# Performance work log

Measured on AMD Instinct MI355X. Metric: run time of the kernel, lower is better.

## Reference

```python
import jax, jax.numpy as jnp
import numpy as np

B, V, F, N = 4, 8192, 16384, 8192
EPS = 1e-3        # criterion eps
WEIGHT = 1000.0   # criterion weight


def setup_inputs() -> dict:
    key = jax.random.key(0)
    k1, k2, k3 = jax.random.split(key, 3)
    pred_pos = jax.random.normal(k1, (B, N, 3), jnp.float32)
    obstacle_pos = jax.random.normal(k2, (B, V, 3), jnp.float32)
    obstacle_faces = jax.random.randint(k3, (B, F, 3), 0, V)
    return {"pred_pos": pred_pos, "obstacle_pos": obstacle_pos,
            "obstacle_faces": obstacle_faces}


def _centers_normals(pos, faces):
    # pos: [V,3], faces: [F,3] -> face centers [F,3], unit face normals [F,3]
    tri = pos[faces]                                   # [F,3,3]
    centers = tri.mean(axis=1)                         # gather(...).mean(-2)
    n = jnp.cross(tri[:, 1] - tri[:, 0], tri[:, 2] - tri[:, 0])
    n = n / jnp.maximum(jnp.linalg.norm(n, axis=-1, keepdims=True), 1e-12)
    return centers, n


def reference(pred_pos, obstacle_pos, obstacle_faces):
    centers, normals = jax.vmap(_centers_normals)(obstacle_pos, obstacle_faces)
    # brute-force 1-NN: argmin_f ||p - c_f||^2 == argmin_f (||c_f||^2 - 2 p.c_f)
    c2 = jnp.sum(centers * centers, axis=-1)                     # [B,F]
    dots = jnp.einsum('bnd,bfd->bnf', pred_pos, centers)         # [B,N,F] big
    nn_idx = jnp.argmin(c2[:, None, :] - 2.0 * dots, axis=-1)    # [B,N]
    idx3 = jnp.broadcast_to(nn_idx[:, :, None], nn_idx.shape + (3,))
    nn_points = jnp.take_along_axis(centers, idx3, axis=1)       # [B,N,3]
    nn_normals = jnp.take_along_axis(normals, idx3, axis=1)      # [B,N,3]
    distance = jnp.sum((pred_pos - nn_points) * nn_normals, axis=-1)  # [B,N]
    interp = jnp.maximum(EPS - distance, 0.0)
    perc = jnp.mean((interp > 0).astype(jnp.float32))            # mean over B of per-example means (equal N)
    loss = jnp.mean(jnp.sum(interp ** 3, axis=-1)) * WEIGHT      # sum_i loss_i / B * weight
    return loss, perc
```

## Files before the change

kernel.cpp:

```cpp
#include <hip/hip_runtime.h>
#include <cstdint>

typedef __attribute__((ext_vector_type(8)))  short short8;
typedef __attribute__((ext_vector_type(16))) float floatx16;

constexpr int NB = 4;
constexpr int NV = 8192;
constexpr int NF = 16384;
constexpr int NP = 8192;
constexpr float F_EPS = 1e-3f;
constexpr float F_WEIGHT = 1000.0f;
constexpr float BIAS = 1e-3f;

constexpr int PT_TILES = NP / 32;
constexpr int FC_TILES = NF / 32;
constexpr int TPB = 256;
constexpr int FS = 16;
constexpr int SL_TILES = FC_TILES / FS;
constexpr int CH = 16;
constexpr int NCHUNK = SL_TILES / CH;
constexpr int PGB = 64;

union FragU { uint4 u; short8 s; };

__device__ inline unsigned f2bf(float f) {
    unsigned u = __float_as_uint(f);
    return (u + 0x7FFFu + ((u >> 16) & 1u)) >> 16;
}
__device__ inline float bf2f(unsigned h) { return __uint_as_float(h << 16); }
__device__ inline unsigned pk(unsigned lo, unsigned hi) {
    return (lo & 0xFFFFu) | (hi << 16);
}

__global__ void prep_kernel(const float* __restrict__ pred,
                            const float* __restrict__ pos,
                            const int*   __restrict__ faces,
                            uint4* __restrict__ a_frags,
                            uint4* __restrict__ b_frags,
                            float4* __restrict__ centers4,
                            float4* __restrict__ normals4,
                            unsigned* __restrict__ keys,
                            float* __restrict__ acc,
                            unsigned* __restrict__ tk) {
    int i = blockIdx.x * blockDim.x + threadIdx.x;
    if (i >= NB * NF) return;
    if (i < 2) acc[i] = 0.0f;
    if (i == 0) tk[0] = 0u;

    const unsigned ONE = 0x3F80u;

    {
        int b = i / NF, f = i & (NF - 1);
        const float* p = pos + (size_t)b * NV * 3;
        int i0 = faces[3 * (size_t)i], i1 = faces[3 * (size_t)i + 1], i2 = faces[3 * (size_t)i + 2];
        float ax = p[3 * i0], ay = p[3 * i0 + 1], az = p[3 * i0 + 2];
        float bx = p[3 * i1], by = p[3 * i1 + 1], bz = p[3 * i1 + 2];
        float cx = p[3 * i2], cy = p[3 * i2 + 1], cz = p[3 * i2 + 2];

        const float third = 1.0f / 3.0f;
        float mx = (ax + bx + cx) * third;
        float my = (ay + by + cy) * third;
        float mz = (az + bz + cz) * third;
        float c2 = mx * mx + my * my + mz * mz;

        float e1x = bx - ax, e1y = by - ay, e1z = bz - az;
        float e2x = cx - ax, e2y = cy - ay, e2z = cz - az;
        float nx = e1y * e2z - e1z * e2y;
        float ny = e1z * e2x - e1x * e2z;
        float nz = e1x * e2y - e1y * e2x;
        float len = sqrtf(nx * nx + ny * ny + nz * nz);
        float inv = 1.0f / fmaxf(len, 1e-12f);

        centers4[i] = make_float4(mx, my, mz, c2);
        normals4[i] = make_float4(nx * inv, ny * inv, nz * inv, 0.0f);

        unsigned bhx = f2bf(mx), bhy = f2bf(my), bhz = f2bf(mz);
        unsigned blx = f2bf(mx - bf2f(bhx)), bly = f2bf(my - bf2f(bhy)), blz = f2bf(mz - bf2f(bhz));
        unsigned c2h = f2bf(c2);
        unsigned c2l = f2bf(c2 - bf2f(c2h));

        int tile = f >> 5, n = f & 31;
        uint4* bb = b_frags + (size_t)(b * FC_TILES + tile) * 64;
        bb[n]      = make_uint4(pk(bhx, bhy), pk(bhz, bhx), pk(bhy, bhz), pk(blx, bly));
        bb[32 + n] = make_uint4(pk(blz, blx), pk(bly, blz), pk(c2h, c2l), pk(ONE, ONE));
    }

    if (i < NB * NP) {
        keys[i] = 0xFFFFFFFFu;
        int pb = i / NP, pn = i & (NP - 1);
        float x = pred[3 * (size_t)i], y = pred[3 * (size_t)i + 1], z = pred[3 * (size_t)i + 2];
        unsigned hx = f2bf(x), hy = f2bf(y), hz = f2bf(z);
        float rx = x - bf2f(hx), ry = y - bf2f(hy), rz = z - bf2f(hz);
        unsigned ahx = f2bf(-2.f * bf2f(hx)), ahy = f2bf(-2.f * bf2f(hy)), ahz = f2bf(-2.f * bf2f(hz));
        unsigned alx = f2bf(-2.f * rx), aly = f2bf(-2.f * ry), alz = f2bf(-2.f * rz);
        float p2 = x * x + y * y + z * z + BIAS;
        unsigned p2h = f2bf(p2);
        unsigned p2l = f2bf(p2 - bf2f(p2h));

        int tile = pn >> 5, m = pn & 31;
        uint4* ab = a_frags + (size_t)(pb * PT_TILES + tile) * 64;
        ab[m]      = make_uint4(pk(ahx, ahy), pk(ahz, alx), pk(aly, alz), pk(ahx, ahy));
        ab[32 + m] = make_uint4(pk(ahz, alx), pk(aly, alz), pk(ONE, ONE), pk(p2h, p2l));
    }
}

__global__ __launch_bounds__(TPB) void nn_kernel(
        const uint4* __restrict__ a_frags,
        const uint4* __restrict__ b_frags,
        unsigned* __restrict__ keys) {
    const int pg = blockIdx.x, sl = blockIdx.y, b = blockIdx.z;
    const int tid = threadIdx.x, wave = tid >> 6, lane = tid & 63;

    __shared__ uint4 sb[CH * 64];

    const int pt_tile = pg * 4 + wave;
    FragU a;
    a.u = a_frags[((size_t)(b * PT_TILES + pt_tile)) * 64 + lane];

    unsigned best[16];
#pragma unroll
    for (int e = 0; e < 16; ++e) best[e] = 0xFFFFFFFFu;

    const floatx16 zero = {0.f, 0.f, 0.f, 0.f, 0.f, 0.f, 0.f, 0.f,
                           0.f, 0.f, 0.f, 0.f, 0.f, 0.f, 0.f, 0.f};
    const uint4* bp = b_frags + ((size_t)(b * FC_TILES + sl * SL_TILES)) * 64;

    for (int ch = 0; ch < NCHUNK; ++ch) {
        const uint4* gsrc = bp + (size_t)ch * CH * 64;
        __syncthreads();
#pragma unroll
        for (int k = 0; k < (CH * 64) / TPB; ++k)
            sb[k * TPB + tid] = gsrc[k * TPB + tid];
        __syncthreads();

        unsigned vf = (unsigned)((sl * SL_TILES + ch * CH) * 32 + (lane & 31));
#pragma unroll
        for (int t = 0; t < CH; t += 2) {
            FragU fb0, fb1;
            fb0.u = sb[t * 64 + lane];
            fb1.u = sb[t * 64 + 64 + lane];
            floatx16 d0, d1;
            asm("v_mfma_f32_32x32x16_bf16 %0, %2, %3, %5\n\t"
                "v_mfma_f32_32x32x16_bf16 %1, %2, %4, %5\n\t"
                "s_nop 7\n\t"
                "s_nop 7"
                : "=&v"(d0), "=&v"(d1)
                : "v"(a.s), "v"(fb0.s), "v"(fb1.s), "v"(zero));
#pragma unroll
            for (int r = 0; r < 16; ++r) {
                unsigned k0 = (__float_as_uint(d0[r]) & 0xFFFFC000u) | vf;
                unsigned k1 = (__float_as_uint(d1[r]) & 0xFFFFC000u) | (vf + 32u);
                best[r] = min(best[r], min(k0, k1));
            }
            vf += 64u;
        }
    }

#pragma unroll
    for (int e = 0; e < 16; ++e) {
        unsigned v = best[e];
#pragma unroll
        for (int m = 1; m < 32; m <<= 1)
            v = min(v, (unsigned)__shfl_xor((int)v, m, 64));
        best[e] = v;
    }
    unsigned* kb = keys + b * NP;
    if ((lane & 31) == 0) {
        int half = lane >> 5;
#pragma unroll
        for (int r = 0; r < 16; ++r) {
            int row = (r & 3) + 8 * (r >> 2) + 4 * half;
            atomicMin(&kb[pt_tile * 32 + row], best[r]);
        }
    }
}

__global__ __launch_bounds__(TPB) void finalize_kernel(
        const float* __restrict__ pred,
        const float4* __restrict__ centers4,
        const float4* __restrict__ normals4,
        const unsigned int* __restrict__ keys,
        float* __restrict__ acc,
        unsigned* __restrict__ tk,
        float* __restrict__ out,
        int nblocks) {
    int i = blockIdx.x * blockDim.x + threadIdx.x;
    float val = 0.0f, cnt = 0.0f;
    if (i < NB * NP) {
        int b = i / NP;
        unsigned key = keys[i];
        int idx = (int)(key & (unsigned)(NF - 1));
        float4 c  = centers4[b * NF + idx];
        float4 nr = normals4[b * NF + idx];
        const float* pp = pred + (size_t)i * 3;
        float dx = pp[0] - c.x, dy = pp[1] - c.y, dz = pp[2] - c.z;
        float dist = dx * nr.x + dy * nr.y + dz * nr.z;
        float t = F_EPS - dist;
        if (t > 0.0f) { cnt = 1.0f; val = t * t * t; }
    }
    for (int off = 32; off > 0; off >>= 1) {
        val += __shfl_down(val, off, 64);
        cnt += __shfl_down(cnt, off, 64);
    }
    __shared__ float sv[TPB / 64], sn[TPB / 64];
    __shared__ unsigned s_tkt;
    int lane = threadIdx.x & 63, wave = threadIdx.x >> 6;
    if (lane == 0) { sv[wave] = val; sn[wave] = cnt; }
    __syncthreads();
    if (threadIdx.x == 0) {
        float v = 0.0f, cc = 0.0f;
#pragma unroll
        for (int w = 0; w < TPB / 64; ++w) { v += sv[w]; cc += sn[w]; }
        atomicAdd(&acc[0], v);
        atomicAdd(&acc[1], cc);
        __threadfence();
        s_tkt = atomicAdd(&tk[0], 1u);
        if (s_tkt == (unsigned)(nblocks - 1)) {
            float a0 = __hip_atomic_load(&acc[0], __ATOMIC_RELAXED, __HIP_MEMORY_SCOPE_AGENT);
            float a1 = __hip_atomic_load(&acc[1], __ATOMIC_RELAXED, __HIP_MEMORY_SCOPE_AGENT);
            out[0] = a0 * (F_WEIGHT / (float)NB);
            out[1] = a1 * (1.0f / (float)(NB * NP));
        }
    }
}

extern "C" void kernel_launch(void* const* d_in, const int* in_sizes, int n_in,
                              void* d_out, int out_size, void* d_ws, size_t ws_size,
                              hipStream_t stream) {
    const float* pred  = (const float*)d_in[0];
    const float* opos  = (const float*)d_in[1];
    const int*   faces = (const int*)  d_in[2];

    char* ws = (char*)d_ws;
    const size_t a_bytes = (size_t)NB * PT_TILES * 64 * 16;
    const size_t b_bytes = (size_t)NB * FC_TILES * 64 * 16;
    const size_t c_bytes = (size_t)NB * NF * 16;
    const size_t k_bytes = (size_t)NB * NP * sizeof(unsigned);

    uint4*    a_frags  = (uint4*)ws;
    uint4*    b_frags  = (uint4*)(ws + a_bytes);
    float4*   centers4 = (float4*)(ws + a_bytes + b_bytes);
    float4*   normals4 = (float4*)(ws + a_bytes + b_bytes + c_bytes);
    unsigned* keys     = (unsigned*)(ws + a_bytes + b_bytes + 2 * c_bytes);
    float*    acc      = (float*)(ws + a_bytes + b_bytes + 2 * c_bytes + k_bytes);
    unsigned* tk       = (unsigned*)(ws + a_bytes + b_bytes + 2 * c_bytes + k_bytes + 64);

    prep_kernel<<<(NB * NF + TPB - 1) / TPB, TPB, 0, stream>>>(
        pred, opos, faces, a_frags, b_frags, centers4, normals4, keys, acc, tk);

    nn_kernel<<<dim3(PGB, FS, NB), TPB, 0, stream>>>(a_frags, b_frags, keys);

    int fin_blocks = (NB * NP + TPB - 1) / TPB;
    finalize_kernel<<<fin_blocks, TPB, 0, stream>>>(
        pred, centers4, normals4, keys, acc, tk, (float*)d_out, fin_blocks);
}
```

Measured before the change: 113.2 us.

## Load whole face slice into LDS once and hand-schedule MFMA loop in asm

Replaces the chunked LDS staging loop, which had two barriers per chunk, with a single up-front load of the block's entire face slice (32 tiles, 32KB) into shared memory. The compute loop is rewritten as one inline-asm block that does explicit ds_read_b128 loads, paired MFMAs, and a fused v_and_or/v_min3 epilogue on fixed registers. This removes repeated barriers and lets the epilogue use min3, but it serialises each LDS read behind an lgkmcnt(0) wait with no software pipelining. The larger LDS allocation may also reduce the number of blocks resident per CU.

```diff
diff --git a/kernel.cpp b/kernel.cpp
--- a/kernel.cpp
+++ b/kernel.cpp
@@ -17,8 +17,6 @@
 constexpr int TPB = 256;
 constexpr int FS = 16;
 constexpr int SL_TILES = FC_TILES / FS;
-constexpr int CH = 16;
-constexpr int NCHUNK = SL_TILES / CH;
 constexpr int PGB = 64;
 
 union FragU { uint4 u; short8 s; };
@@ -104,6 +102,31 @@
     }
 }
 
+#define EP(D0, D1, BB) \
+    "v_and_or_b32 v56, " D0 ", %[m], v58\n\t" \
+    "v_and_or_b32 v57, " D1 ", %[m], v60\n\t" \
+    "v_min3_u32 " BB ", " BB ", v56, v57\n\t"
+
+#define PAIR(O0, O1) \
+    "ds_read_b128 v[48:51], v59 offset:" O0 "\n\t" \
+    "ds_read_b128 v[52:55], v59 offset:" O1 "\n\t" \
+    "s_waitcnt lgkmcnt(0)\n\t" \
+    "v_mfma_f32_32x32x16_bf16 v[0:15], %[fa], v[48:51], %[fz]\n\t" \
+    "v_mfma_f32_32x32x16_bf16 v[16:31], %[fa], v[52:55], %[fz]\n\t" \
+    "v_add_u32 v60, 32, v58\n\t" \
+    "s_nop 7\n\t" \
+    "s_nop 7\n\t" \
+    "s_nop 7\n\t" \
+    EP("v0",  "v16", "v32") EP("v1",  "v17", "v33") \
+    EP("v2",  "v18", "v34") EP("v3",  "v19", "v35") \
+    EP("v4",  "v20", "v36") EP("v5",  "v21", "v37") \
+    EP("v6",  "v22", "v38") EP("v7",  "v23", "v39") \
+    EP("v8",  "v24", "v40") EP("v9",  "v25", "v41") \
+    EP("v10", "v26", "v42") EP("v11", "v27", "v43") \
+    EP("v12", "v28", "v44") EP("v13", "v29", "v45") \
+    EP("v14", "v30", "v46") EP("v15", "v31", "v47") \
+    "v_add_u32 v58, 64, v58\n\t"
+
 __global__ __launch_bounds__(TPB) void nn_kernel(
         const uint4* __restrict__ a_frags,
         const uint4* __restrict__ b_frags,
@@ -111,50 +134,77 @@
     const int pg = blockIdx.x, sl = blockIdx.y, b = blockIdx.z;
     const int tid = threadIdx.x, wave = tid >> 6, lane = tid & 63;
 
-    __shared__ uint4 sb[CH * 64];
+    __shared__ uint4 sb[SL_TILES * 64];
 
     const int pt_tile = pg * 4 + wave;
     FragU a;
     a.u = a_frags[((size_t)(b * PT_TILES + pt_tile)) * 64 + lane];
 
-    unsigned best[16];
-#pragma unroll
-    for (int e = 0; e < 16; ++e) best[e] = 0xFFFFFFFFu;
+    const uint4* gsrc = b_frags + ((size_t)(b * FC_TILES + sl * SL_TILES)) * 64;
+#pragma unroll
+    for (int k = 0; k < (SL_TILES * 64) / TPB; ++k)
+        sb[k * TPB + tid] = gsrc[k * TPB + tid];
+    __syncthreads();
 
     const floatx16 zero = {0.f, 0.f, 0.f, 0.f, 0.f, 0.f, 0.f, 0.f,
                            0.f, 0.f, 0.f, 0.f, 0.f, 0.f, 0.f, 0.f};
-    const uint4* bp = b_frags + ((size_t)(b * FC_TILES + sl * SL_TILES)) * 64;
-
-    for (int ch = 0; ch < NCHUNK; ++ch) {
-        const uint4* gsrc = bp + (size_t)ch * CH * 64;
-        __syncthreads();
-#pragma unroll
-        for (int k = 0; k < (CH * 64) / TPB; ++k)
-            sb[k * TPB + tid] = gsrc[k * TPB + tid];
-        __syncthreads();
-
-        unsigned vf = (unsigned)((sl * SL_TILES + ch * CH) * 32 + (lane & 31));
-#pragma unroll
-        for (int t = 0; t < CH; t += 2) {
-            FragU fb0, fb1;
-            fb0.u = sb[t * 64 + lane];
-            fb1.u = sb[t * 64 + 64 + lane];
-            floatx16 d0, d1;
-            asm("v_mfma_f32_32x32x16_bf16 %0, %2, %3, %5\n\t"
-                "v_mfma_f32_32x32x16_bf16 %1, %2, %4, %5\n\t"
-                "s_nop 7\n\t"
-                "s_nop 7"
-                : "=&v"(d0), "=&v"(d1)
-                : "v"(a.s), "v"(fb0.s), "v"(fb1.s), "v"(zero));
-#pragma unroll
-            for (int r = 0; r < 16; ++r) {
-                unsigned k0 = (__float_as_uint(d0[r]) & 0xFFFFC000u) | vf;
-                unsigned k1 = (__float_as_uint(d1[r]) & 0xFFFFC000u) | (vf + 32u);
-                best[r] = min(best[r], min(k0, k1));
-            }
-            vf += 64u;
-        }
-    }
+    const unsigned mask = 0xFFFFC000u;
+    const unsigned vf_base = (unsigned)(sl * (SL_TILES * 32) + (lane & 31));
+    const unsigned lds_base = (unsigned)(unsigned long long)&sb[lane];
+
+    unsigned b0, b1, b2, b3, b4, b5, b6, b7, b8, b9, b10, b11, b12, b13, b14, b15;
+    asm volatile(
+        "v_mov_b32 v59, %[lb]\n\t"
+        "v_mov_b32 v58, %[vfb]\n\t"
+        "v_mov_b32 v32, -1\n\t" "v_mov_b32 v33, -1\n\t"
+        "v_mov_b32 v34, -1\n\t" "v_mov_b32 v35, -1\n\t"
+        "v_mov_b32 v36, -1\n\t" "v_mov_b32 v37, -1\n\t"
+        "v_mov_b32 v38, -1\n\t" "v_mov_b32 v39, -1\n\t"
+        "v_mov_b32 v40, -1\n\t" "v_mov_b32 v41, -1\n\t"
+        "v_mov_b32 v42, -1\n\t" "v_mov_b32 v43, -1\n\t"
+        "v_mov_b32 v44, -1\n\t" "v_mov_b32 v45, -1\n\t"
+        "v_mov_b32 v46, -1\n\t" "v_mov_b32 v47, -1\n\t"
+        PAIR("0",     "1024")
+        PAIR("2048",  "3072")
+        PAIR("4096",  "5120")
+        PAIR("6144",  "7168")
+        PAIR("8192",  "9216")
+        PAIR("10240", "11264")
+        PAIR("12288", "13312")
+        PAIR("14336", "15360")
+        PAIR("16384", "17408")
+        PAIR("18432", "19456")
+        PAIR("20480", "21504")
+        PAIR("22528", "23552")
+        PAIR("24576", "25600")
+        PAIR("26624", "27648")
+        PAIR("28672", "29696")
+        PAIR("30720", "31744")
+        "v_mov_b32 %0, v32\n\t"  "v_mov_b32 %1, v33\n\t"
+        "v_mov_b32 %2, v34\n\t"  "v_mov_b32 %3, v35\n\t"
+        "v_mov_b32 %4, v36\n\t"  "v_mov_b32 %5, v37\n\t"
+        "v_mov_b32 %6, v38\n\t"  "v_mov_b32 %7, v39\n\t"
+        "v_mov_b32 %8, v40\n\t"  "v_mov_b32 %9, v41\n\t"
+        "v_mov_b32 %10, v42\n\t" "v_mov_b32 %11, v43\n\t"
+        "v_mov_b32 %12, v44\n\t" "v_mov_b32 %13, v45\n\t"
+        "v_mov_b32 %14, v46\n\t" "v_mov_b32 %15, v47"
+        : "=v"(b0), "=v"(b1), "=v"(b2), "=v"(b3),
+          "=v"(b4), "=v"(b5), "=v"(b6), "=v"(b7),
+          "=v"(b8), "=v"(b9), "=v"(b10), "=v"(b11),
+          "=v"(b12), "=v"(b13), "=v"(b14), "=v"(b15)
+        : [fa]"v"(a.s), [fz]"v"(zero), [m]"s"(mask),
+          [vfb]"v"(vf_base), [lb]"v"(lds_base)
+        : "v0","v1","v2","v3","v4","v5","v6","v7",
+          "v8","v9","v10","v11","v12","v13","v14","v15",
+          "v16","v17","v18","v19","v20","v21","v22","v23",
+          "v24","v25","v26","v27","v28","v29","v30","v31",
+          "v32","v33","v34","v35","v36","v37","v38","v39",
+          "v40","v41","v42","v43","v44","v45","v46","v47",
+          "v48","v49","v50","v51","v52","v53","v54","v55",
+          "v56","v57","v58","v59","v60","memory");
+
+    unsigned best[16] = {b0, b1, b2, b3, b4, b5, b6, b7,
+                         b8, b9, b10, b11, b12, b13, b14, b15};
 
 #pragma unroll
     for (int e = 0; e < 16; ++e) {
```

Result: faster. 105.5 us (-6.9%).

## Hand-schedule NN MFMA loop in asm with whole-slice LDS and per-slice key buffers

Applied to the files above, without the earlier changes.

Each block now loads its whole face slice into LDS once with global_load_lds, replacing the chunked loop that synchronised per chunk. Each wave processes two point tiles per B fragment, and the MFMA + key-min epilogue is written in inline assembly with double-buffered ds_reads and v_min3/and_or fusion. Cross-lane reduction uses DPP and swizzle. Atomics are replaced by per-slice key stores that finalize min-reduces over 16 slices. Risks: large LDS footprint (32KB) and fixed register clobbers reduce occupancy, plus extra finalize reads.

```diff
diff --git a/kernel.cpp b/kernel.cpp
--- a/kernel.cpp
+++ b/kernel.cpp
@@ -17,9 +17,8 @@
 constexpr int TPB = 256;
 constexpr int FS = 16;
 constexpr int SL_TILES = FC_TILES / FS;
-constexpr int CH = 16;
-constexpr int NCHUNK = SL_TILES / CH;
-constexpr int PGB = 64;
+constexpr int GPW = 2;
+constexpr int PGB = 16;
 
 union FragU { uint4 u; short8 s; };
 
@@ -39,7 +38,6 @@
                             uint4* __restrict__ b_frags,
                             float4* __restrict__ centers4,
                             float4* __restrict__ normals4,
-                            unsigned* __restrict__ keys,
                             float* __restrict__ acc,
                             unsigned* __restrict__ tk) {
     int i = blockIdx.x * blockDim.x + threadIdx.x;
@@ -86,7 +84,6 @@
     }
 
     if (i < NB * NP) {
-        keys[i] = 0xFFFFFFFFu;
         int pb = i / NP, pn = i & (NP - 1);
         float x = pred[3 * (size_t)i], y = pred[3 * (size_t)i + 1], z = pred[3 * (size_t)i + 2];
         unsigned hx = f2bf(x), hy = f2bf(y), hz = f2bf(z);
@@ -104,74 +101,202 @@
     }
 }
 
+#define EP(D0, D1, BB) \
+    "v_and_or_b32 v80, " D0 ", %[m], v82\n\t" \
+    "v_and_or_b32 v81, " D1 ", %[m], v83\n\t" \
+    "v_min3_u32 " BB ", " BB ", v80, v81\n\t"
+
+#define EP0_ALL \
+    EP("v0","v16","v32") EP("v1","v17","v33") EP("v2","v18","v34") EP("v3","v19","v35") \
+    EP("v4","v20","v36") EP("v5","v21","v37") EP("v6","v22","v38") EP("v7","v23","v39") \
+    EP("v8","v24","v40") EP("v9","v25","v41") EP("v10","v26","v42") EP("v11","v27","v43") \
+    EP("v12","v28","v44") EP("v13","v29","v45") EP("v14","v30","v46") EP("v15","v31","v47")
+
+#define EP1_ALL \
+    EP("v0","v16","v48") EP("v1","v17","v49") EP("v2","v18","v50") EP("v3","v19","v51") \
+    EP("v4","v20","v52") EP("v5","v21","v53") EP("v6","v22","v54") EP("v7","v23","v55") \
+    EP("v8","v24","v56") EP("v9","v25","v57") EP("v10","v26","v58") EP("v11","v27","v59") \
+    EP("v12","v28","v60") EP("v13","v29","v61") EP("v14","v30","v62") EP("v15","v31","v63")
+
+#define BODY_X \
+    "s_waitcnt lgkmcnt(2)\n\t" \
+    "v_mfma_f32_32x32x16_bf16 v[0:15], %[fa0], v[64:67], %[fz]\n\t" \
+    "v_mfma_f32_32x32x16_bf16 v[16:31], %[fa0], v[68:71], %[fz]\n\t" \
+    "v_add_u32 v83, 32, v82\n\t" \
+    "s_nop 7\n\t" "s_nop 7\n\t" "s_nop 7\n\t" \
+    EP0_ALL \
+    "v_mfma_f32_32x32x16_bf16 v[0:15], %[fa1], v[64:67], %[fz]\n\t" \
+    "v_mfma_f32_32x32x16_bf16 v[16:31], %[fa1], v[68:71], %[fz]\n\t" \
+    "s_nop 7\n\t" "s_nop 7\n\t" "s_nop 7\n\t" \
+    EP1_ALL \
+    "v_add_u32 v82, 64, v82\n\t"
+
+#define BODY_Y \
+    "s_waitcnt lgkmcnt(2)\n\t" \
+    "v_mfma_f32_32x32x16_bf16 v[0:15], %[fa0], v[72:75], %[fz]\n\t" \
+    "v_mfma_f32_32x32x16_bf16 v[16:31], %[fa0], v[76:79], %[fz]\n\t" \
+    "v_add_u32 v83, 32, v82\n\t" \
+    "s_nop 7\n\t" "s_nop 7\n\t" "s_nop 7\n\t" \
+    EP0_ALL \
+    "v_mfma_f32_32x32x16_bf16 v[0:15], %[fa1], v[72:75], %[fz]\n\t" \
+    "v_mfma_f32_32x32x16_bf16 v[16:31], %[fa1], v[76:79], %[fz]\n\t" \
+    "s_nop 7\n\t" "s_nop 7\n\t" "s_nop 7\n\t" \
+    EP1_ALL \
+    "v_add_u32 v82, 64, v82\n\t"
+
+#define ITER_X(P0, P1) \
+    "ds_read_b128 v[72:75], v84 offset:" P0 "\n\t" \
+    "ds_read_b128 v[76:79], v84 offset:" P1 "\n\t" \
+    BODY_X
+#define ITER_Y(P0, P1) \
+    "ds_read_b128 v[64:67], v84 offset:" P0 "\n\t" \
+    "ds_read_b128 v[68:71], v84 offset:" P1 "\n\t" \
+    BODY_Y
+#define ITER_Y_LAST \
+    "s_waitcnt lgkmcnt(1)\n\t" \
+    "v_mfma_f32_32x32x16_bf16 v[0:15], %[fa0], v[72:75], %[fz]\n\t" \
+    "s_waitcnt lgkmcnt(0)\n\t" \
+    "v_mfma_f32_32x32x16_bf16 v[16:31], %[fa0], v[76:79], %[fz]\n\t" \
+    "v_add_u32 v83, 32, v82\n\t" \
+    "s_nop 7\n\t" "s_nop 7\n\t" "s_nop 7\n\t" \
+    EP0_ALL \
+    "v_mfma_f32_32x32x16_bf16 v[0:15], %[fa1], v[72:75], %[fz]\n\t" \
+    "v_mfma_f32_32x32x16_bf16 v[16:31], %[fa1], v[76:79], %[fz]\n\t" \
+    "s_nop 7\n\t" "s_nop 7\n\t" "s_nop 7\n\t" \
+    EP1_ALL
+
+#define DPP1(R, S) "v_min_u32_dpp v" R ", v" R ", v" R " row_ror:" S " row_mask:0xf bank_mask:0xf\n\t"
+#define DPPS(S) \
+    DPP1("32",S) DPP1("33",S) DPP1("34",S) DPP1("35",S) DPP1("36",S) DPP1("37",S) \
+    DPP1("38",S) DPP1("39",S) DPP1("40",S) DPP1("41",S) DPP1("42",S) DPP1("43",S) \
+    DPP1("44",S) DPP1("45",S) DPP1("46",S) DPP1("47",S) DPP1("48",S) DPP1("49",S) \
+    DPP1("50",S) DPP1("51",S) DPP1("52",S) DPP1("53",S) DPP1("54",S) DPP1("55",S) \
+    DPP1("56",S) DPP1("57",S) DPP1("58",S) DPP1("59",S) DPP1("60",S) DPP1("61",S) \
+    DPP1("62",S) DPP1("63",S)
+
+#define SWZ(D, S) "ds_swizzle_b32 v" D ", v" S " offset:0x401F\n\t"
+#define MN(A, B)  "v_min_u32 v" A ", v" A ", v" B "\n\t"
+#define ST(R, OFF) "global_store_dword %[kb], v" R ", off offset:" OFF "\n\t"
+
 __global__ __launch_bounds__(TPB) void nn_kernel(
         const uint4* __restrict__ a_frags,
         const uint4* __restrict__ b_frags,
-        unsigned* __restrict__ keys) {
+        unsigned* __restrict__ skeys) {
     const int pg = blockIdx.x, sl = blockIdx.y, b = blockIdx.z;
     const int tid = threadIdx.x, wave = tid >> 6, lane = tid & 63;
 
-    __shared__ uint4 sb[CH * 64];
-
-    const int pt_tile = pg * 4 + wave;
-    FragU a;
-    a.u = a_frags[((size_t)(b * PT_TILES + pt_tile)) * 64 + lane];
-
-    unsigned best[16];
+    __shared__ uint4 sb[SL_TILES * 64];
+
+    const uint4* gsrc = b_frags + ((size_t)(b * FC_TILES + sl * SL_TILES)) * 64;
 #pragma unroll
-    for (int e = 0; e < 16; ++e) best[e] = 0xFFFFFFFFu;
+    for (int k = 0; k < (SL_TILES * 64) / TPB; ++k) {
+        __builtin_amdgcn_global_load_lds(
+            (const __attribute__((address_space(1))) unsigned int*)(const void*)(gsrc + k * TPB + tid),
+            (__attribute__((address_space(3))) unsigned int*)(void*)&sb[k * TPB + (wave << 6)],
+            16, 0, 0);
+    }
+    __syncthreads();
 
     const floatx16 zero = {0.f, 0.f, 0.f, 0.f, 0.f, 0.f, 0.f, 0.f,
                            0.f, 0.f, 0.f, 0.f, 0.f, 0.f, 0.f, 0.f};
-    const uint4* bp = b_frags + ((size_t)(b * FC_TILES + sl * SL_TILES)) * 64;
-
-    for (int ch = 0; ch < NCHUNK; ++ch) {
-        const uint4* gsrc = bp + (size_t)ch * CH * 64;
-        __syncthreads();
-#pragma unroll
-        for (int k = 0; k < (CH * 64) / TPB; ++k)
-            sb[k * TPB + tid] = gsrc[k * TPB + tid];
-        __syncthreads();
-
-        unsigned vf = (unsigned)((sl * SL_TILES + ch * CH) * 32 + (lane & 31));
-#pragma unroll
-        for (int t = 0; t < CH; t += 2) {
-            FragU fb0, fb1;
-            fb0.u = sb[t * 64 + lane];
-            fb1.u = sb[t * 64 + 64 + lane];
-            floatx16 d0, d1;
-            asm("v_mfma_f32_32x32x16_bf16 %0, %2, %3, %5\n\t"
-                "v_mfma_f32_32x32x16_bf16 %1, %2, %4, %5\n\t"
-                "s_nop 7\n\t"
-                "s_nop 7"
-                : "=&v"(d0), "=&v"(d1)
-                : "v"(a.s), "v"(fb0.s), "v"(fb1.s), "v"(zero));
-#pragma unroll
-            for (int r = 0; r < 16; ++r) {
-                unsigned k0 = (__float_as_uint(d0[r]) & 0xFFFFC000u) | vf;
-                unsigned k1 = (__float_as_uint(d1[r]) & 0xFFFFC000u) | (vf + 32u);
-                best[r] = min(best[r], min(k0, k1));
-            }
-            vf += 64u;
-        }
-    }
-
-#pragma unroll
-    for (int e = 0; e < 16; ++e) {
-        unsigned v = best[e];
-#pragma unroll
-        for (int m = 1; m < 32; m <<= 1)
-            v = min(v, (unsigned)__shfl_xor((int)v, m, 64));
-        best[e] = v;
-    }
-    unsigned* kb = keys + b * NP;
-    if ((lane & 31) == 0) {
-        int half = lane >> 5;
-#pragma unroll
-        for (int r = 0; r < 16; ++r) {
-            int row = (r & 3) + 8 * (r >> 2) + 4 * half;
-            atomicMin(&kb[pt_tile * 32 + row], best[r]);
-        }
+    const unsigned mask = 0xFFFFC000u;
+    const unsigned vf_base = (unsigned)(sl * (SL_TILES * 32) + (lane & 31));
+    const unsigned lds_base = (unsigned)(unsigned long long)&sb[lane];
+    const unsigned act = ((lane & 31) == 0) ? 1u : 0u;
+    unsigned* skb = skeys + ((size_t)(b * FS + sl)) * NP;
+
+#pragma unroll 1
+    for (int g = 0; g < GPW; ++g) {
+        const int pt0 = pg * 16 + g * 8 + wave * 2;
+        FragU a0, a1;
+        a0.u = a_frags[((size_t)(b * PT_TILES + pt0)) * 64 + lane];
+        a1.u = a_frags[((size_t)(b * PT_TILES + pt0 + 1)) * 64 + lane];
+        unsigned long long kaddr =
+            (unsigned long long)(skb + pt0 * 32 + ((lane >> 5) * 4));
+        unsigned long long saved;
+
+        asm volatile(
+            "v_mov_b32 v84, %[lb]\n\t"
+            "v_mov_b32 v82, %[vfb]\n\t"
+            "v_mov_b32 v32, -1\n\t" "v_mov_b32 v33, -1\n\t"
+            "v_mov_b32 v34, -1\n\t" "v_mov_b32 v35, -1\n\t"
+            "v_mov_b32 v36, -1\n\t" "v_mov_b32 v37, -1\n\t"
+            "v_mov_b32 v38, -1\n\t" "v_mov_b32 v39, -1\n\t"
+            "v_mov_b32 v40, -1\n\t" "v_mov_b32 v41, -1\n\t"
+            "v_mov_b32 v42, -1\n\t" "v_mov_b32 v43, -1\n\t"
+            "v_mov_b32 v44, -1\n\t" "v_mov_b32 v45, -1\n\t"
+            "v_mov_b32 v46, -1\n\t" "v_mov_b32 v47, -1\n\t"
+            "v_mov_b32 v48, -1\n\t" "v_mov_b32 v49, -1\n\t"
+            "v_mov_b32 v50, -1\n\t" "v_mov_b32 v51, -1\n\t"
+            "v_mov_b32 v52, -1\n\t" "v_mov_b32 v53, -1\n\t"
+            "v_mov_b32 v54, -1\n\t" "v_mov_b32 v55, -1\n\t"
+            "v_mov_b32 v56, -1\n\t" "v_mov_b32 v57, -1\n\t"
+            "v_mov_b32 v58, -1\n\t" "v_mov_b32 v59, -1\n\t"
+            "v_mov_b32 v60, -1\n\t" "v_mov_b32 v61, -1\n\t"
+            "v_mov_b32 v62, -1\n\t" "v_mov_b32 v63, -1\n\t"
+            "ds_read_b128 v[64:67], v84 offset:0\n\t"
+            "ds_read_b128 v[68:71], v84 offset:1024\n\t"
+            ITER_X("2048",  "3072")
+            ITER_Y("4096",  "5120")
+            ITER_X("6144",  "7168")
+            ITER_Y("8192",  "9216")
+            ITER_X("10240", "11264")
+            ITER_Y("12288", "13312")
+            ITER_X("14336", "15360")
+            ITER_Y("16384", "17408")
+            ITER_X("18432", "19456")
+            ITER_Y("20480", "21504")
+            ITER_X("22528", "23552")
+            ITER_Y("24576", "25600")
+            ITER_X("26624", "27648")
+            ITER_Y("28672", "29696")
+            ITER_X("30720", "31744")
+            ITER_Y_LAST
+            "s_nop 1\n\t"
+            DPPS("1") DPPS("2") DPPS("4") DPPS("8")
+            SWZ("0","32") SWZ("1","33") SWZ("2","34") SWZ("3","35")
+            SWZ("4","36") SWZ("5","37") SWZ("6","38") SWZ("7","39")
+            SWZ("8","40") SWZ("9","41") SWZ("10","42") SWZ("11","43")
+            SWZ("12","44") SWZ("13","45") SWZ("14","46") SWZ("15","47")
+            SWZ("16","48") SWZ("17","49") SWZ("18","50") SWZ("19","51")
+            SWZ("20","52") SWZ("21","53") SWZ("22","54") SWZ("23","55")
+            SWZ("24","56") SWZ("25","57") SWZ("26","58") SWZ("27","59")
+            SWZ("28","60") SWZ("29","61") SWZ("30","62") SWZ("31","63")
+            "s_waitcnt lgkmcnt(0)\n\t"
+            MN("32","0") MN("33","1") MN("34","2") MN("35","3")
+            MN("36","4") MN("37","5") MN("38","6") MN("39","7")
+            MN("40","8") MN("41","9") MN("42","10") MN("43","11")
+            MN("44","12") MN("45","13") MN("46","14") MN("47","15")
+            MN("48","16") MN("49","17") MN("50","18") MN("51","19")
+            MN("52","20") MN("53","21") MN("54","22") MN("55","23")
+            MN("56","24") MN("57","25") MN("58","26") MN("59","27")
+            MN("60","28") MN("61","29") MN("62","30") MN("63","31")
+            "v_cmp_eq_u32 vcc, 1, %[act]\n\t"
+            "s_and_saveexec_b64 %[sv], vcc\n\t"
+            ST("32","0")   ST("33","4")   ST("34","8")   ST("35","12")
+            ST("36","32")  ST("37","36")  ST("38","40")  ST("39","44")
+            ST("40","64")  ST("41","68")  ST("42","72")  ST("43","76")
+            ST("44","96")  ST("45","100") ST("46","104") ST("47","108")
+            ST("48","128") ST("49","132") ST("50","136") ST("51","140")
+            ST("52","160") ST("53","164") ST("54","168") ST("55","172")
+            ST("56","192") ST("57","196") ST("58","200") ST("59","204")
+            ST("60","224") ST("61","228") ST("62","232") ST("63","236")
+            "s_mov_b64 exec, %[sv]"
+            : [sv]"=&s"(saved)
+            : [fa0]"v"(a0.s), [fa1]"v"(a1.s), [fz]"v"(zero), [m]"s"(mask),
+              [vfb]"v"(vf_base), [lb]"v"(lds_base), [act]"v"(act),
+              [kb]"v"(kaddr)
+            : "v0","v1","v2","v3","v4","v5","v6","v7",
+              "v8","v9","v10","v11","v12","v13","v14","v15",
+              "v16","v17","v18","v19","v20","v21","v22","v23",
+              "v24","v25","v26","v27","v28","v29","v30","v31",
+              "v32","v33","v34","v35","v36","v37","v38","v39",
+              "v40","v41","v42","v43","v44","v45","v46","v47",
+              "v48","v49","v50","v51","v52","v53","v54","v55",
+              "v56","v57","v58","v59","v60","v61","v62","v63",
+              "v64","v65","v66","v67","v68","v69","v70","v71",
+              "v72","v73","v74","v75","v76","v77","v78","v79",
+              "v80","v81","v82","v83","v84","vcc","scc","memory");
     }
 }
 
@@ -179,7 +304,7 @@
         const float* __restrict__ pred,
         const float4* __restrict__ centers4,
         const float4* __restrict__ normals4,
-        const unsigned int* __restrict__ keys,
+        const unsigned* __restrict__ skeys,
         float* __restrict__ acc,
         unsigned* __restrict__ tk,
         float* __restrict__ out,
@@ -187,8 +312,11 @@
     int i = blockIdx.x * blockDim.x + threadIdx.x;
     float val = 0.0f, cnt = 0.0f;
     if (i < NB * NP) {
-        int b = i / NP;
-        unsigned key = keys[i];
+        int b = i / NP, n = i & (NP - 1);
+        unsigned key = 0xFFFFFFFFu;
+#pragma unroll
+        for (int s = 0; s < FS; ++s)
+            key = min(key, skeys[((size_t)(b * FS + s)) * NP + n]);
         int idx = (int)(key & (unsigned)(NF - 1));
         float4 c  = centers4[b * NF + idx];
         float4 nr = normals4[b * NF + idx];
@@ -235,22 +363,22 @@
     const size_t a_bytes = (size_t)NB * PT_TILES * 64 * 16;
     const size_t b_bytes = (size_t)NB * FC_TILES * 64 * 16;
     const size_t c_bytes = (size_t)NB * NF * 16;
-    const size_t k_bytes = (size_t)NB * NP * sizeof(unsigned);
+    const size_t s_bytes = (size_t)NB * FS * NP * 4;
 
     uint4*    a_frags  = (uint4*)ws;
     uint4*    b_frags  = (uint4*)(ws + a_bytes);
     float4*   centers4 = (float4*)(ws + a_bytes + b_bytes);
     float4*   normals4 = (float4*)(ws + a_bytes + b_bytes + c_bytes);
-    unsigned* keys     = (unsigned*)(ws + a_bytes + b_bytes + 2 * c_bytes);
-    float*    acc      = (float*)(ws + a_bytes + b_bytes + 2 * c_bytes + k_bytes);
-    unsigned* tk       = (unsigned*)(ws + a_bytes + b_bytes + 2 * c_bytes + k_bytes + 64);
+    unsigned* skeys    = (unsigned*)(ws + a_bytes + b_bytes + 2 * c_bytes);
+    float*    acc      = (float*)(ws + a_bytes + b_bytes + 2 * c_bytes + s_bytes);
+    unsigned* tk       = (unsigned*)(ws + a_bytes + b_bytes + 2 * c_bytes + s_bytes + 64);
 
     prep_kernel<<<(NB * NF + TPB - 1) / TPB, TPB, 0, stream>>>(
-        pred, opos, faces, a_frags, b_frags, centers4, normals4, keys, acc, tk);
-
-    nn_kernel<<<dim3(PGB, FS, NB), TPB, 0, stream>>>(a_frags, b_frags, keys);
+        pred, opos, faces, a_frags, b_frags, centers4, normals4, acc, tk);
+
+    nn_kernel<<<dim3(PGB, FS, NB), TPB, 0, stream>>>(a_frags, b_frags, skeys);
 
     int fin_blocks = (NB * NP + TPB - 1) / TPB;
     finalize_kernel<<<fin_blocks, TPB, 0, stream>>>(
-        pred, centers4, normals4, keys, acc, tk, (float*)d_out, fin_blocks);
-}
+        pred, centers4, normals4, skeys, acc, tk, (float*)d_out, fin_blocks);
+}
```

New measurement: 104.5 us. 1.08x faster.
